# Optimization experiments

Measured on AMD Instinct MI355X. Metric: run time of the kernel, lower is better.

Reference implementation:

```python
import jax, jax.numpy as jnp
import numpy as np

B, L = 512, 200
WORD_V, PATH_V = 100000, 200000
E, D = 128, 384


def setup_inputs() -> dict:
    key = jax.random.key(0)
    ks = jax.random.split(key, 10)
    inp = {
        "x_s1": jax.random.randint(ks[0], (B, L), 0, WORD_V),
        "path1": jax.random.randint(ks[1], (B, L), 0, PATH_V),
        "x_t1": jax.random.randint(ks[2], (B, L), 0, WORD_V),
        "x_s2": jax.random.randint(ks[3], (B, L), 0, WORD_V),
        "path2": jax.random.randint(ks[4], (B, L), 0, PATH_V),
        "x_t2": jax.random.randint(ks[5], (B, L), 0, WORD_V),
        # learned parameters
        "word_emb": jax.random.normal(ks[6], (WORD_V, E), dtype=jnp.float32) * 0.02,
        "path_emb": jax.random.normal(ks[7], (PATH_V, E), dtype=jnp.float32) * 0.02,
        "W_fc": jax.random.normal(ks[8], (D, 3 * E), dtype=jnp.float32) * (1.0 / np.sqrt(3 * E)),  # nn.Linear weight [out, in], no bias
        "attn": jax.random.uniform(ks[9], (D, 1), dtype=jnp.float32),
    }
    return inp


def _extract(xs, path, xt, word_emb, path_emb, W_fc, attn):
    # gather + concat -> [B, L, 3E]
    ctx = jnp.concatenate([word_emb[xs], path_emb[path], word_emb[xt]], axis=-1)
    # linear (no bias, dropout is identity at eval) + tanh -> [B, L, D]
    h = jnp.tanh(jnp.einsum('blf,df->bld', ctx, W_fc))
    # attention scores [B, L, 1]; the zeros mask in the original is a no-op
    scores = jnp.einsum('bld,do->blo', h, attn)
    a = jax.nn.softmax(scores, axis=1)
    code_vec = jnp.sum(h * a, axis=1)  # [B, D]
    return code_vec, a


def reference(x_s1, path1, x_t1, x_s2, path2, x_t2, word_emb, path_emb, W_fc, attn):
    cv1, _ = _extract(x_s1, path1, x_t1, word_emb, path_emb, W_fc, attn)
    cv2, _ = _extract(x_s2, path2, x_t2, word_emb, path_emb, W_fc, attn)
    return (cv1, cv2)
```

## Files before the change

### kernel.cpp

```cpp
#include <hip/hip_runtime.h>
#include <hip/hip_bf16.h>

#define B_N 512
#define L_N 200
#define E_N 128
#define K_N 384
#define D_N 384
#define ASTR 392

typedef __bf16 v8bf  __attribute__((ext_vector_type(8)));
typedef float  v4f   __attribute__((ext_vector_type(4)));
typedef unsigned int v4u __attribute__((ext_vector_type(4)));

__device__ __forceinline__ unsigned short f2bf(float f) {
    union { __bf16 b; unsigned short u; } cv;
    cv.b = (__bf16)f;
    return cv.u;
}
__device__ __forceinline__ float fast_tanh(float x) {
    float e = __expf(2.f * x);
    return 1.f - 2.f / (e + 1.f);
}

__global__ void pack_w(const float* __restrict__ W, unsigned short* __restrict__ Wp) {
    int gid  = blockIdx.x * 256 + threadIdx.x;
    int lane = gid & 63;
    int u    = gid >> 6;
    int gn   = u % 24;
    int kk   = u / 24;
    int c    = lane & 15, quad = lane >> 4;
    const float* src = W + (gn * 16 + c) * K_N + kk * 32 + quad * 8;
    ushort4 lo, hi;
    lo.x = f2bf(src[0]); lo.y = f2bf(src[1]); lo.z = f2bf(src[2]); lo.w = f2bf(src[3]);
    hi.x = f2bf(src[4]); hi.y = f2bf(src[5]); hi.z = f2bf(src[6]); hi.w = f2bf(src[7]);
    ushort4* dst = (ushort4*)(Wp + (size_t)gid * 8);
    dst[0] = lo; dst[1] = hi;
}

__global__ __launch_bounds__(512, 4)
void c2v_fused(const int* __restrict__ xs1, const int* __restrict__ ph1,
               const int* __restrict__ xt1,
               const int* __restrict__ xs2, const int* __restrict__ ph2,
               const int* __restrict__ xt2,
               const float* __restrict__ wemb, const float* __restrict__ pemb,
               const unsigned short* __restrict__ Wp,
               const float* __restrict__ attn,
               float* __restrict__ out)
{
    const int tid  = threadIdx.x;
    const int wv   = tid >> 6;
    const int lane = tid & 63;
    const int quad = lane >> 4;
    const int c    = lane & 15;
    const int b    = blockIdx.x;
    const int pass = blockIdx.y;

    const int* xs = pass ? xs2 : xs1;
    const int* ph = pass ? ph2 : ph1;
    const int* xt = pass ? xt2 : xt1;

    __shared__ unsigned short Alds[64 * ASTR];
    __shared__ float sp[8][64];
    __shared__ float alds[68];
    __shared__ int   ilds[3 * 208];

    for (int u = tid; u < 624; u += 512) {
        int s = u / 208, g = u - s * 208;
        const int* tab = (s == 0) ? xs : (s == 1) ? ph : xt;
        ilds[u] = (g < L_N) ? tab[b * L_N + g] : 0;
    }

    const float an0 = attn[(wv * 3 + 0) * 16 + c];
    const float an1 = attn[(wv * 3 + 1) * 16 + c];
    const float an2 = attn[(wv * 3 + 2) * 16 + c];

    float o0 = 0.f, o1 = 0.f, o2 = 0.f;
    float Mrun = -1e30f, Zrun = 0.f;

    const v4u* wp4 = (const v4u*)Wp;

    for (int chunk = 0; chunk < 4; ++chunk) {
        const int row0 = chunk * 64;

        v4f acc[4][3];
        #pragma unroll
        for (int i = 0; i < 4; ++i)
            #pragma unroll
            for (int j = 0; j < 3; ++j)
                acc[i][j] = (v4f){0.f, 0.f, 0.f, 0.f};

        __syncthreads();

        #pragma unroll 2
        for (int i = 0; i < 6; ++i) {
            int u = i * 512 + tid;
            int s = u >> 10;
            int r = u & 1023;
            int m = r >> 4;
            int j = r & 15;
            int g = row0 + m;
            ushort4 lo, hi;
            if (g < L_N) {
                const float* ebase = (s == 1) ? pemb : wemb;
                const float* src = ebase + (size_t)ilds[s * 208 + g] * E_N + j * 8;
                const float4 f0 = *(const float4*)(src);
                const float4 f1 = *(const float4*)(src + 4);
                lo.x = f2bf(f0.x); lo.y = f2bf(f0.y); lo.z = f2bf(f0.z); lo.w = f2bf(f0.w);
                hi.x = f2bf(f1.x); hi.y = f2bf(f1.y); hi.z = f2bf(f1.z); hi.w = f2bf(f1.w);
            } else {
                lo.x = lo.y = lo.z = lo.w = 0;
                hi.x = hi.y = hi.z = hi.w = 0;
            }
            ushort4* dst = (ushort4*)&Alds[m * ASTR + s * 128 + j * 8];
            dst[0] = lo; dst[1] = hi;
        }
        __syncthreads();

        #pragma unroll 2
        for (int kk = 0; kk < 12; ++kk) {
            v8bf b0 = __builtin_bit_cast(v8bf, wp4[(kk * 24 + wv * 3 + 0) * 64 + lane]);
            v8bf b1 = __builtin_bit_cast(v8bf, wp4[(kk * 24 + wv * 3 + 1) * 64 + lane]);
            v8bf b2 = __builtin_bit_cast(v8bf, wp4[(kk * 24 + wv * 3 + 2) * 64 + lane]);
            #pragma unroll
            for (int mt = 0; mt < 4; ++mt) {
                v8bf a = *(const v8bf*)&Alds[(mt * 16 + c) * ASTR + kk * 32 + quad * 8];
                acc[mt][0] = __builtin_amdgcn_mfma_f32_16x16x32_bf16(a, b0, acc[mt][0], 0, 0, 0);
                acc[mt][1] = __builtin_amdgcn_mfma_f32_16x16x32_bf16(a, b1, acc[mt][1], 0, 0, 0);
                acc[mt][2] = __builtin_amdgcn_mfma_f32_16x16x32_bf16(a, b2, acc[mt][2], 0, 0, 0);
            }
        }

        #pragma unroll
        for (int mt = 0; mt < 4; ++mt) {
            #pragma unroll
            for (int r = 0; r < 4; ++r) {
                float h0 = fast_tanh(acc[mt][0][r]);
                float h1 = fast_tanh(acc[mt][1][r]);
                float h2 = fast_tanh(acc[mt][2][r]);
                acc[mt][0][r] = h0; acc[mt][1][r] = h1; acc[mt][2][r] = h2;
                float sv = h0 * an0 + h1 * an1 + h2 * an2;
                sv += __shfl_xor(sv, 1);
                sv += __shfl_xor(sv, 2);
                sv += __shfl_xor(sv, 4);
                sv += __shfl_xor(sv, 8);
                if (c == 0) sp[wv][mt * 16 + quad * 4 + r] = sv;
            }
        }
        __syncthreads();

        if (wv == 0) {
            int g = row0 + lane;
            float s = sp[0][lane] + sp[1][lane] + sp[2][lane] + sp[3][lane]
                    + sp[4][lane] + sp[5][lane] + sp[6][lane] + sp[7][lane];
            if (g >= L_N) s = -1e30f;
            float mx = s;
            #pragma unroll
            for (int off = 32; off > 0; off >>= 1) mx = fmaxf(mx, __shfl_xor(mx, off));
            float Mnew  = fmaxf(Mrun, mx);
            float alpha = __expf(Mrun - Mnew);
            float e = (g < L_N) ? __expf(s - Mnew) : 0.f;
            float zc = e;
            #pragma unroll
            for (int off = 32; off > 0; off >>= 1) zc += __shfl_xor(zc, off);
            Zrun = Zrun * alpha + zc;
            Mrun = Mnew;
            alds[lane] = e;
            if (lane == 0) alds[64] = alpha;
        }
        __syncthreads();

        const float al = alds[64];
        float p0 = 0.f, p1 = 0.f, p2 = 0.f;
        #pragma unroll
        for (int mt = 0; mt < 4; ++mt) {
            #pragma unroll
            for (int r = 0; r < 4; ++r) {
                float w = alds[mt * 16 + quad * 4 + r];
                p0 += w * acc[mt][0][r];
                p1 += w * acc[mt][1][r];
                p2 += w * acc[mt][2][r];
            }
        }
        o0 = o0 * al + p0;
        o1 = o1 * al + p1;
        o2 = o2 * al + p2;
    }

    if (tid == 0) alds[65] = Zrun;
    __syncthreads();
    const float zinv = 1.f / alds[65];

    float* outp = out + (size_t)(pass * B_N + b) * D_N;
    o0 += __shfl_xor(o0, 16); o0 += __shfl_xor(o0, 32);
    o1 += __shfl_xor(o1, 16); o1 += __shfl_xor(o1, 32);
    o2 += __shfl_xor(o2, 16); o2 += __shfl_xor(o2, 32);
    if (quad == 0) {
        outp[(wv * 3 + 0) * 16 + c] = o0 * zinv;
        outp[(wv * 3 + 1) * 16 + c] = o1 * zinv;
        outp[(wv * 3 + 2) * 16 + c] = o2 * zinv;
    }
}

extern "C" void kernel_launch(void* const* d_in, const int* in_sizes, int n_in,
                              void* d_out, int out_size, void* d_ws, size_t ws_size,
                              hipStream_t stream) {
    unsigned short* Wp = (unsigned short*)d_ws;
    pack_w<<<72, 256, 0, stream>>>((const float*)d_in[8], Wp);
    dim3 grid(B_N, 2, 1);
    c2v_fused<<<grid, 512, 0, stream>>>(
        (const int*)d_in[0], (const int*)d_in[1], (const int*)d_in[2],
        (const int*)d_in[3], (const int*)d_in[4], (const int*)d_in[5],
        (const float*)d_in[6], (const float*)d_in[7],
        Wp, (const float*)d_in[9],
        (float*)d_out);
}
```

Measured before the change: 307.2 us.

## Prefetch next chunk's embedding gathers into registers during MFMA; trim last chunk

Embedding rows for the next 64-row chunk are loaded into registers while the current chunk's MFMA and tanh work runs, instead of being loaded right before use. The goal is to hide gather latency behind compute. The final chunk now computes only the 16 rows it actually has rather than 64 padded rows. tanh and the final normalisation use the hardware reciprocal instead of a division. The 48 extra float registers for the prefetch buffers may hurt occupancy under the 512x4 launch bounds or cause spills.

After: 406.4 us. +32.3%, slower.

```diff
diff --git a/kernel.cpp b/kernel.cpp
--- a/kernel.cpp
+++ b/kernel.cpp
@@ -11,6 +11,7 @@
 typedef __bf16 v8bf  __attribute__((ext_vector_type(8)));
 typedef float  v4f   __attribute__((ext_vector_type(4)));
 typedef unsigned int v4u __attribute__((ext_vector_type(4)));
+typedef unsigned short v8us __attribute__((ext_vector_type(8)));
 
 __device__ __forceinline__ unsigned short f2bf(float f) {
     union { __bf16 b; unsigned short u; } cv;
@@ -19,7 +20,7 @@
 }
 __device__ __forceinline__ float fast_tanh(float x) {
     float e = __expf(2.f * x);
-    return 1.f - 2.f / (e + 1.f);
+    return 1.f - 2.f * __builtin_amdgcn_rcpf(e + 1.f);
 }
 
 __global__ void pack_w(const float* __restrict__ W, unsigned short* __restrict__ Wp) {
@@ -35,6 +36,44 @@
     hi.x = f2bf(src[4]); hi.y = f2bf(src[5]); hi.z = f2bf(src[6]); hi.w = f2bf(src[7]);
     ushort4* dst = (ushort4*)(Wp + (size_t)gid * 8);
     dst[0] = lo; dst[1] = hi;
+}
+
+template<int MT>
+__device__ __forceinline__ void compute_chunk(
+    const unsigned short* Alds, const v4u* wp4, float (*sp)[64],
+    int wv, int lane, int quad, int c,
+    float an0, float an1, float an2,
+    v4f (&acc)[4][3])
+{
+    #pragma unroll 2
+    for (int kk = 0; kk < 12; ++kk) {
+        v8bf b0 = __builtin_bit_cast(v8bf, wp4[(kk * 24 + wv * 3 + 0) * 64 + lane]);
+        v8bf b1 = __builtin_bit_cast(v8bf, wp4[(kk * 24 + wv * 3 + 1) * 64 + lane]);
+        v8bf b2 = __builtin_bit_cast(v8bf, wp4[(kk * 24 + wv * 3 + 2) * 64 + lane]);
+        #pragma unroll
+        for (int mt = 0; mt < MT; ++mt) {
+            v8bf a = *(const v8bf*)&Alds[(mt * 16 + c) * ASTR + kk * 32 + quad * 8];
+            acc[mt][0] = __builtin_amdgcn_mfma_f32_16x16x32_bf16(a, b0, acc[mt][0], 0, 0, 0);
+            acc[mt][1] = __builtin_amdgcn_mfma_f32_16x16x32_bf16(a, b1, acc[mt][1], 0, 0, 0);
+            acc[mt][2] = __builtin_amdgcn_mfma_f32_16x16x32_bf16(a, b2, acc[mt][2], 0, 0, 0);
+        }
+    }
+    #pragma unroll
+    for (int mt = 0; mt < MT; ++mt) {
+        #pragma unroll
+        for (int r = 0; r < 4; ++r) {
+            float h0 = fast_tanh(acc[mt][0][r]);
+            float h1 = fast_tanh(acc[mt][1][r]);
+            float h2 = fast_tanh(acc[mt][2][r]);
+            acc[mt][0][r] = h0; acc[mt][1][r] = h1; acc[mt][2][r] = h2;
+            float sv = h0 * an0 + h1 * an1 + h2 * an2;
+            sv += __shfl_xor(sv, 1);
+            sv += __shfl_xor(sv, 2);
+            sv += __shfl_xor(sv, 4);
+            sv += __shfl_xor(sv, 8);
+            if (c == 0) sp[wv][mt * 16 + quad * 4 + r] = sv;
+        }
+    }
 }
 
 __global__ __launch_bounds__(512, 4)
@@ -79,8 +118,61 @@
 
     const v4u* wp4 = (const v4u*)Wp;
 
+    float4 f0[6], f1[6];
+
+    auto issue = [&](int nc) {
+        const int r0 = nc * 64;
+        const int mr = (nc == 3) ? 16 : 64;
+        #pragma unroll
+        for (int i = 0; i < 6; ++i) {
+            int u = i * 512 + tid;
+            int s = u >> 10;
+            int rr = u & 1023;
+            int m = rr >> 4;
+            int j = rr & 15;
+            int g = r0 + m;
+            if (m < mr && g < L_N) {
+                const float* eb = (s == 1) ? pemb : wemb;
+                const float* src = eb + (size_t)ilds[s * 208 + g] * E_N + j * 8;
+                f0[i] = *(const float4*)src;
+                f1[i] = *(const float4*)(src + 4);
+            }
+        }
+    };
+
+    __syncthreads();
+    issue(0);
+
     for (int chunk = 0; chunk < 4; ++chunk) {
-        const int row0 = chunk * 64;
+        const int row0  = chunk * 64;
+        const int mrows = (chunk == 3) ? 16 : 64;
+        const int mtmax = (chunk == 3) ? 1 : 4;
+
+        v8us cv[6];
+        #pragma unroll
+        for (int i = 0; i < 6; ++i) {
+            int u = i * 512 + tid;
+            int m = (u & 1023) >> 4;
+            int g = row0 + m;
+            bool act = (m < mrows) && (g < L_N);
+            float4 a0 = f0[i], a1 = f1[i];
+            if (!act) { a0.x = a0.y = a0.z = a0.w = 0.f; a1 = a0; }
+            cv[i][0] = f2bf(a0.x); cv[i][1] = f2bf(a0.y);
+            cv[i][2] = f2bf(a0.z); cv[i][3] = f2bf(a0.w);
+            cv[i][4] = f2bf(a1.x); cv[i][5] = f2bf(a1.y);
+            cv[i][6] = f2bf(a1.z); cv[i][7] = f2bf(a1.w);
+        }
+
+        __syncthreads();
+
+        #pragma unroll
+        for (int i = 0; i < 6; ++i) {
+            int u = i * 512 + tid;
+            int s = u >> 10, rr = u & 1023, m = rr >> 4, j = rr & 15;
+            if (m < mrows)
+                *(v8us*)&Alds[m * ASTR + s * 128 + j * 8] = cv[i];
+        }
+        __syncthreads();
 
         v4f acc[4][3];
         #pragma unroll
@@ -89,62 +181,11 @@
             for (int j = 0; j < 3; ++j)
                 acc[i][j] = (v4f){0.f, 0.f, 0.f, 0.f};
 
-        __syncthreads();
-
-        #pragma unroll 2
-        for (int i = 0; i < 6; ++i) {
-            int u = i * 512 + tid;
-            int s = u >> 10;
-            int r = u & 1023;
-            int m = r >> 4;
-            int j = r & 15;
-            int g = row0 + m;
-            ushort4 lo, hi;
-            if (g < L_N) {
-                const float* ebase = (s == 1) ? pemb : wemb;
-                const float* src = ebase + (size_t)ilds[s * 208 + g] * E_N + j * 8;
-                const float4 f0 = *(const float4*)(src);
-                const float4 f1 = *(const float4*)(src + 4);
-                lo.x = f2bf(f0.x); lo.y = f2bf(f0.y); lo.z = f2bf(f0.z); lo.w = f2bf(f0.w);
-                hi.x = f2bf(f1.x); hi.y = f2bf(f1.y); hi.z = f2bf(f1.z); hi.w = f2bf(f1.w);
-            } else {
-                lo.x = lo.y = lo.z = lo.w = 0;
-                hi.x = hi.y = hi.z = hi.w = 0;
-            }
-            ushort4* dst = (ushort4*)&Alds[m * ASTR + s * 128 + j * 8];
-            dst[0] = lo; dst[1] = hi;
-        }
-        __syncthreads();
-
-        #pragma unroll 2
-        for (int kk = 0; kk < 12; ++kk) {
-            v8bf b0 = __builtin_bit_cast(v8bf, wp4[(kk * 24 + wv * 3 + 0) * 64 + lane]);
-            v8bf b1 = __builtin_bit_cast(v8bf, wp4[(kk * 24 + wv * 3 + 1) * 64 + lane]);
-            v8bf b2 = __builtin_bit_cast(v8bf, wp4[(kk * 24 + wv * 3 + 2) * 64 + lane]);
-            #pragma unroll
-            for (int mt = 0; mt < 4; ++mt) {
-                v8bf a = *(const v8bf*)&Alds[(mt * 16 + c) * ASTR + kk * 32 + quad * 8];
-                acc[mt][0] = __builtin_amdgcn_mfma_f32_16x16x32_bf16(a, b0, acc[mt][0], 0, 0, 0);
-                acc[mt][1] = __builtin_amdgcn_mfma_f32_16x16x32_bf16(a, b1, acc[mt][1], 0, 0, 0);
-                acc[mt][2] = __builtin_amdgcn_mfma_f32_16x16x32_bf16(a, b2, acc[mt][2], 0, 0, 0);
-            }
-        }
-
-        #pragma unroll
-        for (int mt = 0; mt < 4; ++mt) {
-            #pragma unroll
-            for (int r = 0; r < 4; ++r) {
-                float h0 = fast_tanh(acc[mt][0][r]);
-                float h1 = fast_tanh(acc[mt][1][r]);
-                float h2 = fast_tanh(acc[mt][2][r]);
-                acc[mt][0][r] = h0; acc[mt][1][r] = h1; acc[mt][2][r] = h2;
-                float sv = h0 * an0 + h1 * an1 + h2 * an2;
-                sv += __shfl_xor(sv, 1);
-                sv += __shfl_xor(sv, 2);
-                sv += __shfl_xor(sv, 4);
-                sv += __shfl_xor(sv, 8);
-                if (c == 0) sp[wv][mt * 16 + quad * 4 + r] = sv;
-            }
+        if (chunk < 3) {
+            compute_chunk<4>(Alds, wp4, sp, wv, lane, quad, c, an0, an1, an2, acc);
+            issue(chunk + 1);
+        } else {
+            compute_chunk<1>(Alds, wp4, sp, wv, lane, quad, c, an0, an1, an2, acc);
         }
         __syncthreads();
 
@@ -173,12 +214,14 @@
         float p0 = 0.f, p1 = 0.f, p2 = 0.f;
         #pragma unroll
         for (int mt = 0; mt < 4; ++mt) {
-            #pragma unroll
-            for (int r = 0; r < 4; ++r) {
-                float w = alds[mt * 16 + quad * 4 + r];
-                p0 += w * acc[mt][0][r];
-                p1 += w * acc[mt][1][r];
-                p2 += w * acc[mt][2][r];
+            if (mt < mtmax) {
+                #pragma unroll
+                for (int r = 0; r < 4; ++r) {
+                    float w = alds[mt * 16 + quad * 4 + r];
+                    p0 += w * acc[mt][0][r];
+                    p1 += w * acc[mt][1][r];
+                    p2 += w * acc[mt][2][r];
+                }
             }
         }
         o0 = o0 * al + p0;
@@ -188,7 +231,7 @@
 
     if (tid == 0) alds[65] = Zrun;
     __syncthreads();
-    const float zinv = 1.f / alds[65];
+    const float zinv = __builtin_amdgcn_rcpf(alds[65]);
 
     float* outp = out + (size_t)(pass * B_N + b) * D_N;
     o0 += __shfl_xor(o0, 16); o0 += __shfl_xor(o0, 32);
```
